# Performance work log

Hardware: AMD Instinct MI355X
Metric: run time of the kernel (lower is better)

The kernel has to match this reference:

```python
import jax, jax.numpy as jnp
import numpy as np

H = 1024      # hidden_size
I = 2048      # intermediate_size
E = 32        # num_routed_experts
B, S = 4, 2048


def setup_inputs() -> dict:
    key = jax.random.key(0)
    ks = jax.random.split(key, 8)
    scale = 0.02
    inp = {
        "hidden_states": jax.random.normal(ks[0], (B, S, H), dtype=jnp.float32),
        # router gate: stored [H, E] so logits = x @ gate_w
        "gate_w": jax.random.normal(ks[1], (H, E), dtype=jnp.float32) * scale,
        # shared SwiGLU (num_shared_experts=1), weights stored [in, out]
        "shared_gate_w": jax.random.normal(ks[2], (H, I), dtype=jnp.float32) * scale,
        "shared_up_w": jax.random.normal(ks[3], (H, I), dtype=jnp.float32) * scale,
        "shared_down_w": jax.random.normal(ks[4], (I, H), dtype=jnp.float32) * scale,
        # routed grouped SwiGLU, weights stored [E, in, out] (matches GroupedLinear)
        "routed_gate_w": jax.random.normal(ks[5], (E, H, I), dtype=jnp.float32) * scale,
        "routed_up_w": jax.random.normal(ks[6], (E, H, I), dtype=jnp.float32) * scale,
        "routed_down_w": jax.random.normal(ks[7], (E, I, H), dtype=jnp.float32) * scale,
    }
    return inp


def _grouped_mm(a, w, group_sizes):
    # a: [T, in], w: [E, in, out], group_sizes: [E] int32 -> [T, out]
    return jax.lax.ragged_dot(a, w, group_sizes)


def _swiglu(x, gw, uw, dw):
    return (jax.nn.silu(x @ gw) * (x @ uw)) @ dw


def reference(hidden_states, gate_w, shared_gate_w, shared_up_w, shared_down_w,
              routed_gate_w, routed_up_w, routed_down_w):
    b, s, h = hidden_states.shape
    x = hidden_states.reshape(-1, h)                      # [T, H]

    # ---- shared expert ----
    shared_out = _swiglu(x, shared_gate_w, shared_up_w, shared_down_w)

    # ---- router: top-1 ----
    logits = x @ gate_w                                   # [T, E]
    topk_ids = jnp.argmax(logits, axis=-1)                # [T]
    topk_val = jnp.max(logits, axis=-1)                   # [T]
    scores = jax.nn.sigmoid(topk_val)[:, None]            # [T, 1]
    xs = x * scores                                       # scale tokens by router score

    # ---- dispatch: sort tokens by expert id ----
    tokens_per_expert = jnp.zeros((E,), jnp.int32).at[topk_ids].add(1)
    order = jnp.argsort(topk_ids)                         # token ids sorted by expert
    sorted_x = xs[order]                                  # [T, H]

    # ---- grouped SwiGLU experts ----
    g = _grouped_mm(sorted_x, routed_gate_w, tokens_per_expert)   # [T, I]
    u = _grouped_mm(sorted_x, routed_up_w, tokens_per_expert)     # [T, I]
    d = _grouped_mm(jax.nn.silu(g) * u, routed_down_w, tokens_per_expert)  # [T, H]

    # ---- combine: unsort back to token order ----
    inv = jnp.argsort(order)
    routed_out = d[inv]

    return (shared_out + routed_out).reshape(b, s, h)
```

## Files before the change

kernel.cpp:

```cpp
#include <hip/hip_runtime.h>
#include <stdint.h>
#include <stddef.h>

#define TOK 8192
#define H 1024
#define IDIM 2048
#define NE 32
#define BM 128
#define BK 64
#define MAX_TILES 96

typedef __attribute__((ext_vector_type(8))) short short8;
typedef __attribute__((ext_vector_type(4))) float f32x4;
typedef __attribute__((ext_vector_type(4))) float float4v;
typedef __attribute__((ext_vector_type(4))) unsigned int uint4v;


__device__ __forceinline__ unsigned short f2bf(float x) {
  unsigned u = __builtin_bit_cast(unsigned, x);
  u += 0x7fffu + ((u >> 16) & 1u);
  return (unsigned short)(u >> 16);
}

__device__ __forceinline__ unsigned cvtpk(float lo, float hi) {
  unsigned r;
  asm("v_cvt_pk_bf16_f32 %0, %1, %2" : "=v"(r) : "v"(lo), "v"(hi));
  return r;
}

__device__ __forceinline__ void gll16(const void* g, void* l) {
  __builtin_amdgcn_global_load_lds(
      (const __attribute__((address_space(1))) unsigned int*)g,
      (__attribute__((address_space(3))) unsigned int*)l, 16, 0, 0);
}

__device__ __forceinline__ f32x4 mfma16(short8 a, short8 b, f32x4 c) {
  return __builtin_amdgcn_mfma_f32_16x16x32_bf16(a, b, c, 0, 0, 0);
}


__global__ __launch_bounds__(256) void tconv_kernel(
    const float* __restrict__ src0, unsigned short* __restrict__ dst0,
    int K, int N)
{
  __shared__ float t[64][65];
  const size_t mat = (size_t)K * N;
  const float* src = src0 + (size_t)blockIdx.z * mat;
  unsigned short* dst = dst0 + (size_t)blockIdx.z * mat;
  const int k0 = blockIdx.x * 64, n0 = blockIdx.y * 64;
  const int tid = threadIdx.x;
  {
    const int r = tid >> 4;
    const int c = (tid & 15) * 4;
    #pragma unroll
    for (int i = 0; i < 4; ++i) {
      float4v v = *(const float4v*)(src + (size_t)(k0 + r + i * 16) * N + (n0 + c));
      t[r + i * 16][c + 0] = v[0];
      t[r + i * 16][c + 1] = v[1];
      t[r + i * 16][c + 2] = v[2];
      t[r + i * 16][c + 3] = v[3];
    }
  }
  __syncthreads();
  {
    const int n = tid >> 2;
    const int kc = (tid & 3) * 16;
    uint4v o0, o1;
    #pragma unroll
    for (int q = 0; q < 4; ++q) {
      o0[q] = cvtpk(t[kc + 2 * q][n],     t[kc + 2 * q + 1][n]);
      o1[q] = cvtpk(t[kc + 8 + 2 * q][n], t[kc + 8 + 2 * q + 1][n]);
    }
    unsigned short* dp = dst + (size_t)(n0 + n) * K + (k0 + kc);
    *(uint4v*)dp = o0;
    *(uint4v*)(dp + 8) = o1;
  }
}


__global__ __launch_bounds__(256) void router_kernel(
    const float* __restrict__ x, const float* __restrict__ gw,
    unsigned short* __restrict__ xbf, unsigned short* __restrict__ xsbf,
    int* __restrict__ expert_id, int* __restrict__ counts)
{
  __shared__ float xl[8 * H];
  __shared__ float plog[8][8][NE];
  __shared__ float sscore[8];
  const int tid = threadIdx.x;
  const long t0 = (long)blockIdx.x * 8;

  const float4v* src = (const float4v*)(x + t0 * H);
  float4v* dst = (float4v*)xl;
  #pragma unroll
  for (int i = 0; i < 8; ++i) dst[tid + i * 256] = src[tid + i * 256];
  __syncthreads();

  {
    const int e = tid & 31, c = tid >> 5;
    float acc[8] = {0, 0, 0, 0, 0, 0, 0, 0};
    const float* gp = gw + (c * 128) * NE + e;
    for (int h = 0; h < 128; ++h) {
      float g = gp[h * NE];
      const float* xr = xl + (c * 128 + h);
      #pragma unroll
      for (int tk = 0; tk < 8; ++tk) acc[tk] += xr[tk * H] * g;
    }
    #pragma unroll
    for (int tk = 0; tk < 8; ++tk) plog[c][tk][e] = acc[tk];
  }
  __syncthreads();
  {
    const int e = tid & 31, tok = tid >> 5;
    float lg = 0.f;
    #pragma unroll
    for (int c = 0; c < 8; ++c) lg += plog[c][tok][e];
    float m = lg; int be = e;
    #pragma unroll
    for (int mask = 16; mask >= 1; mask >>= 1) {
      float om = __shfl_xor(m, mask);
      int   oe = __shfl_xor(be, mask);
      if (om > m || (om == m && oe < be)) { m = om; be = oe; }
    }
    if (e == 0) {
      sscore[tok] = 1.f / (1.f + __expf(-m));
      expert_id[t0 + tok] = be;
      atomicAdd(&counts[be], 1);
    }
  }
  __syncthreads();
  {
    const float sc = sscore[tid >> 5];
    const int base = (tid >> 5) * H + (tid & 31) * 32;
    #pragma unroll
    for (int i = 0; i < 4; ++i) {
      uint4v vx, vs;
      #pragma unroll
      for (int q = 0; q < 4; ++q) {
        const float a = xl[base + i * 8 + 2 * q];
        const float b = xl[base + i * 8 + 2 * q + 1];
        vx[q] = cvtpk(a, b);
        vs[q] = cvtpk(a * sc, b * sc);
      }
      *(uint4v*)(xbf  + t0 * H + base + i * 8) = vx;
      *(uint4v*)(xsbf + t0 * H + base + i * 8) = vs;
    }
  }
}


__global__ void scan_kernel(const int* __restrict__ counts, int* __restrict__ offsets,
                            int* __restrict__ cursor, int* __restrict__ tile_e,
                            int* __restrict__ tile_p, int* __restrict__ n_tiles)
{
  if (threadIdx.x != 0) return;
  int off = 0, nt = 0;
  for (int e = 0; e < NE; ++e) {
    offsets[e] = off; cursor[e] = off;
    int cc = counts[e];
    for (int k = 0; k < cc; k += BM) { tile_e[nt] = e; tile_p[nt] = off + k; ++nt; }
    off += cc;
  }
  offsets[NE] = off;
  n_tiles[0] = nt;
}


__global__ __launch_bounds__(256) void perm_kernel(
    const int* __restrict__ expert_id, int* __restrict__ cursor, int* __restrict__ perm)
{
  int t = blockIdx.x * 256 + threadIdx.x;
  int e = expert_id[t];
  int pos = atomicAdd(&cursor[e], 1);
  perm[pos] = t;
}


template<bool ROUTED>
__global__ __launch_bounds__(256, 4) void gu_kernel(
    const unsigned short* __restrict__ A,
    const unsigned short* __restrict__ GT,
    const unsigned short* __restrict__ UT,
    unsigned short* __restrict__ act,
    const int* __restrict__ perm, const int* __restrict__ tile_e,
    const int* __restrict__ tile_p, const int* __restrict__ offsets,
    const int* __restrict__ n_tiles)
{
  __shared__ short Al[BM * BK];
  __shared__ short Gl[64 * BK];
  __shared__ short Ul[64 * BK];

  const int tid = threadIdx.x;
  const int wave = tid >> 6, lane = tid & 63;
  const int wm = wave >> 1, wn = wave & 1;

  int row0, row_end;
  const unsigned short *Gt, *Ut;
  if constexpr (ROUTED) {
    if ((int)blockIdx.x >= *n_tiles) return;
    const int e = tile_e[blockIdx.x];
    row0 = tile_p[blockIdx.x];
    row_end = offsets[e + 1];
    Gt = GT + (size_t)e * H * IDIM;
    Ut = UT + (size_t)e * H * IDIM;
  } else {
    row0 = blockIdx.x * BM; row_end = row0 + BM;
    Gt = GT; Ut = UT;
  }
  const int n0 = blockIdx.y * 64;

  const unsigned short* asrc[4];
  int aoff[4];
  #pragma unroll
  for (int i = 0; i < 4; ++i) {
    const int r = wave * 32 + i * 8 + (lane >> 3);
    int p = row0 + r;
    if (ROUTED && p >= row_end) p = row0;
    int arow = p;
    if constexpr (ROUTED) arow = perm[p];
    const int cb = ((lane & 7) * 16) ^ ((r & 7) << 4);
    asrc[i] = A + (size_t)arow * H + (cb >> 1);
    aoff[i] = (wave * 32 + i * 8) * BK;
  }
  const unsigned short *gsrc[2], *usrc[2];
  int boff[2];
  #pragma unroll
  for (int i = 0; i < 2; ++i) {
    const int r = wave * 16 + i * 8 + (lane >> 3);
    const int cb = ((lane & 7) * 16) ^ ((r & 7) << 4);
    gsrc[i] = Gt + (size_t)(n0 + r) * H + (cb >> 1);
    usrc[i] = Ut + (size_t)(n0 + r) * H + (cb >> 1);
    boff[i] = (wave * 16 + i * 8) * BK;
  }

  f32x4 accg[4][2] = {};
  f32x4 accu[4][2] = {};

  #pragma unroll 1
  for (int kt = 0; kt < H / BK; ++kt) {
    __syncthreads();
    #pragma unroll
    for (int i = 0; i < 4; ++i) gll16(asrc[i] + kt * BK, Al + aoff[i]);
    #pragma unroll
    for (int i = 0; i < 2; ++i) gll16(gsrc[i] + kt * BK, Gl + boff[i]);
    #pragma unroll
    for (int i = 0; i < 2; ++i) gll16(usrc[i] + kt * BK, Ul + boff[i]);
    __syncthreads();

    #pragma unroll
    for (int kk = 0; kk < 2; ++kk) {
      short8 af[4];
      #pragma unroll
      for (int m = 0; m < 4; ++m) {
        const int r = wm * 64 + m * 16 + (lane & 15);
        const int cb = (kk * 64 + ((lane >> 4) * 16)) ^ ((r & 7) << 4);
        af[m] = *(const short8*)((const char*)Al + r * 128 + cb);
      }
      #pragma unroll
      for (int nf = 0; nf < 2; ++nf) {
        const int n = wn * 32 + nf * 16 + (lane & 15);
        const int cb = (kk * 64 + ((lane >> 4) * 16)) ^ ((n & 7) << 4);
        short8 bg = *(const short8*)((const char*)Gl + n * 128 + cb);
        short8 bu = *(const short8*)((const char*)Ul + n * 128 + cb);
        #pragma unroll
        for (int m = 0; m < 4; ++m) {
          accg[m][nf] = mfma16(af[m], bg, accg[m][nf]);
          accu[m][nf] = mfma16(af[m], bu, accu[m][nf]);
        }
      }
    }
  }

  #pragma unroll
  for (int m = 0; m < 4; ++m)
    #pragma unroll
    for (int nf = 0; nf < 2; ++nf) {
      const int col = n0 + wn * 32 + nf * 16 + (lane & 15);
      #pragma unroll
      for (int j = 0; j < 4; ++j) {
        const int row = row0 + wm * 64 + m * 16 + ((lane >> 4) * 4) + j;
        if (ROUTED && row >= row_end) continue;
        const float g = accg[m][nf][j];
        const float u = accu[m][nf][j];
        const float v = (g / (1.f + __expf(-g))) * u;
        act[(size_t)row * IDIM + col] = f2bf(v);
      }
    }
}


template<bool ROUTED>
__global__ __launch_bounds__(256, 4) void dn_kernel(
    const unsigned short* __restrict__ A,
    const unsigned short* __restrict__ DT,
    float* __restrict__ out,
    const int* __restrict__ perm, const int* __restrict__ tile_e,
    const int* __restrict__ tile_p, const int* __restrict__ offsets,
    const int* __restrict__ n_tiles)
{
  __shared__ short Al[BM * BK];
  __shared__ short Dl[128 * BK];

  const int tid = threadIdx.x;
  const int wave = tid >> 6, lane = tid & 63;
  const int wm = wave >> 1, wn = wave & 1;

  int row0, row_end;
  const unsigned short* Dt;
  if constexpr (ROUTED) {
    if ((int)blockIdx.x >= *n_tiles) return;
    const int e = tile_e[blockIdx.x];
    row0 = tile_p[blockIdx.x];
    row_end = offsets[e + 1];
    Dt = DT + (size_t)e * H * IDIM;
  } else {
    row0 = blockIdx.x * BM; row_end = row0 + BM;
    Dt = DT;
  }
  const int n0 = blockIdx.y * 128;

  const unsigned short *asrc[4], *dsrc[4];
  int soff[4];
  #pragma unroll
  for (int i = 0; i < 4; ++i) {
    const int r = wave * 32 + i * 8 + (lane >> 3);
    int p = row0 + r;
    if (ROUTED && p >= row_end) p = row0;
    const int cb = ((lane & 7) * 16) ^ ((r & 7) << 4);
    asrc[i] = A  + (size_t)p * IDIM + (cb >> 1);
    dsrc[i] = Dt + (size_t)(n0 + r) * IDIM + (cb >> 1);
    soff[i] = (wave * 32 + i * 8) * BK;
  }

  f32x4 acc[4][4] = {};

  #pragma unroll 1
  for (int kt = 0; kt < IDIM / BK; ++kt) {
    __syncthreads();
    #pragma unroll
    for (int i = 0; i < 4; ++i) gll16(asrc[i] + kt * BK, Al + soff[i]);
    #pragma unroll
    for (int i = 0; i < 4; ++i) gll16(dsrc[i] + kt * BK, Dl + soff[i]);
    __syncthreads();

    #pragma unroll
    for (int kk = 0; kk < 2; ++kk) {
      short8 af[4];
      #pragma unroll
      for (int m = 0; m < 4; ++m) {
        const int r = wm * 64 + m * 16 + (lane & 15);
        const int cb = (kk * 64 + ((lane >> 4) * 16)) ^ ((r & 7) << 4);
        af[m] = *(const short8*)((const char*)Al + r * 128 + cb);
      }
      #pragma unroll
      for (int nf = 0; nf < 4; ++nf) {
        const int n = wn * 64 + nf * 16 + (lane & 15);
        const int cb = (kk * 64 + ((lane >> 4) * 16)) ^ ((n & 7) << 4);
        short8 bd = *(const short8*)((const char*)Dl + n * 128 + cb);
        #pragma unroll
        for (int m = 0; m < 4; ++m) acc[m][nf] = mfma16(af[m], bd, acc[m][nf]);
      }
    }
  }

  #pragma unroll
  for (int m = 0; m < 4; ++m)
    #pragma unroll
    for (int nf = 0; nf < 4; ++nf) {
      const int col = n0 + wn * 64 + nf * 16 + (lane & 15);
      #pragma unroll
      for (int j = 0; j < 4; ++j) {
        const int row = row0 + wm * 64 + m * 16 + ((lane >> 4) * 4) + j;
        const float v = acc[m][nf][j];
        if constexpr (ROUTED) {
          if (row < row_end) {
            const int t = perm[row];
            out[(size_t)t * H + col] += v;
          }
        } else {
          out[(size_t)row * H + col] = v;
        }
      }
    }
}


extern "C" void kernel_launch(void* const* d_in, const int* in_sizes, int n_in,
                              void* d_out, int out_size, void* d_ws, size_t ws_size,
                              hipStream_t stream) {
  (void)in_sizes; (void)n_in; (void)out_size; (void)ws_size;
  const float* x      = (const float*)d_in[0];
  const float* gate_w = (const float*)d_in[1];
  const float* sgw    = (const float*)d_in[2];
  const float* suw    = (const float*)d_in[3];
  const float* sdw    = (const float*)d_in[4];
  const float* rgw    = (const float*)d_in[5];
  const float* ruw    = (const float*)d_in[6];
  const float* rdw    = (const float*)d_in[7];
  float* out = (float*)d_out;

  char* ws = (char*)d_ws;
  unsigned short* xbf  = (unsigned short*)(ws + 0);
  unsigned short* xsbf = (unsigned short*)(ws + 16777216);
  unsigned short* act  = (unsigned short*)(ws + 33554432);
  int* perm      = (int*)(ws + 67108864);
  int* expert_id = (int*)(ws + 67141632);
  int* counts    = (int*)(ws + 67174400);
  int* offsets   = (int*)(ws + 67174528);
  int* cursor    = (int*)(ws + 67174784);
  int* tile_e    = (int*)(ws + 67174912);
  int* tile_p    = (int*)(ws + 67175424);
  int* n_tiles   = (int*)(ws + 67175936);
  unsigned short* rgwT = (unsigned short*)(ws + 68157440);
  unsigned short* ruwT = (unsigned short*)(ws + 202375168);
  unsigned short* rdwT = (unsigned short*)(ws + 336592896);
  unsigned short* sgwT = (unsigned short*)(ws + 470810624);
  unsigned short* suwT = (unsigned short*)(ws + 475004928);
  unsigned short* sdwT = (unsigned short*)(ws + 479199232);

  hipMemsetAsync(counts, 0, NE * sizeof(int), stream);

  router_kernel<<<TOK / 8, 256, 0, stream>>>(x, gate_w, xbf, xsbf, expert_id, counts);
  scan_kernel<<<1, 64, 0, stream>>>(counts, offsets, cursor, tile_e, tile_p, n_tiles);
  perm_kernel<<<TOK / 256, 256, 0, stream>>>(expert_id, cursor, perm);

  tconv_kernel<<<dim3(H / 64, IDIM / 64, 1), 256, 0, stream>>>(sgw, sgwT, H, IDIM);
  tconv_kernel<<<dim3(H / 64, IDIM / 64, 1), 256, 0, stream>>>(suw, suwT, H, IDIM);
  tconv_kernel<<<dim3(IDIM / 64, H / 64, 1), 256, 0, stream>>>(sdw, sdwT, IDIM, H);
  gu_kernel<false><<<dim3(TOK / BM, IDIM / 64), 256, 0, stream>>>(
      xbf, sgwT, suwT, act, perm, tile_e, tile_p, offsets, n_tiles);
  dn_kernel<false><<<dim3(TOK / BM, H / 128), 256, 0, stream>>>(
      act, sdwT, out, perm, tile_e, tile_p, offsets, n_tiles);

  tconv_kernel<<<dim3(H / 64, IDIM / 64, NE), 256, 0, stream>>>(rgw, rgwT, H, IDIM);
  tconv_kernel<<<dim3(H / 64, IDIM / 64, NE), 256, 0, stream>>>(ruw, ruwT, H, IDIM);
  gu_kernel<true><<<dim3(MAX_TILES, IDIM / 64), 256, 0, stream>>>(
      xsbf, rgwT, ruwT, act, perm, tile_e, tile_p, offsets, n_tiles);
  tconv_kernel<<<dim3(IDIM / 64, H / 64, NE), 256, 0, stream>>>(rdw, rdwT, IDIM, H);
  dn_kernel<true><<<dim3(MAX_TILES, H / 128), 256, 0, stream>>>(
      act, rdwT, out, perm, tile_e, tile_p, offsets, n_tiles);
}
```

Measured before the change: 659.4 us.

## Double-buffer LDS tiles in gate/up and down GEMM kernels

Both expert GEMM kernels now keep two LDS buffers and issue the global-to-LDS load for the next K tile before the MFMA work on the current one. This overlaps memory latency with compute and drops one barrier per iteration. In exchange LDS use doubles and the launch-bounds occupancy hint falls from 4 to 2 blocks per CU. Correctness relies on gll16 completing before the single barrier at the end of each iteration.

After: 842.9 us. +27.8%, slower.

```diff
diff --git a/kernel.cpp b/kernel.cpp
--- a/kernel.cpp
+++ b/kernel.cpp
@@ -176,7 +176,7 @@
 
 
 template<bool ROUTED>
-__global__ __launch_bounds__(256, 4) void gu_kernel(
+__global__ __launch_bounds__(256, 2) void gu_kernel(
     const unsigned short* __restrict__ A,
     const unsigned short* __restrict__ GT,
     const unsigned short* __restrict__ UT,
@@ -185,9 +185,9 @@
     const int* __restrict__ tile_p, const int* __restrict__ offsets,
     const int* __restrict__ n_tiles)
 {
-  __shared__ short Al[BM * BK];
-  __shared__ short Gl[64 * BK];
-  __shared__ short Ul[64 * BK];
+  __shared__ short Al[2][BM * BK];
+  __shared__ short Gl[2][64 * BK];
+  __shared__ short Ul[2][64 * BK];
 
   const int tid = threadIdx.x;
   const int wave = tid >> 6, lane = tid & 63;
@@ -235,17 +235,18 @@
   f32x4 accg[4][2] = {};
   f32x4 accu[4][2] = {};
 
-  #pragma unroll 1
-  for (int kt = 0; kt < H / BK; ++kt) {
-    __syncthreads();
-    #pragma unroll
-    for (int i = 0; i < 4; ++i) gll16(asrc[i] + kt * BK, Al + aoff[i]);
-    #pragma unroll
-    for (int i = 0; i < 2; ++i) gll16(gsrc[i] + kt * BK, Gl + boff[i]);
-    #pragma unroll
-    for (int i = 0; i < 2; ++i) gll16(usrc[i] + kt * BK, Ul + boff[i]);
-    __syncthreads();
-
+  auto stage = [&](int kt, int buf) {
+    #pragma unroll
+    for (int i = 0; i < 4; ++i) gll16(asrc[i] + kt * BK, Al[buf] + aoff[i]);
+    #pragma unroll
+    for (int i = 0; i < 2; ++i) gll16(gsrc[i] + kt * BK, Gl[buf] + boff[i]);
+    #pragma unroll
+    for (int i = 0; i < 2; ++i) gll16(usrc[i] + kt * BK, Ul[buf] + boff[i]);
+  };
+  auto compute = [&](int buf) {
+    const char* ab = (const char*)Al[buf];
+    const char* gb = (const char*)Gl[buf];
+    const char* ub = (const char*)Ul[buf];
     #pragma unroll
     for (int kk = 0; kk < 2; ++kk) {
       short8 af[4];
@@ -253,14 +254,14 @@
       for (int m = 0; m < 4; ++m) {
         const int r = wm * 64 + m * 16 + (lane & 15);
         const int cb = (kk * 64 + ((lane >> 4) * 16)) ^ ((r & 7) << 4);
-        af[m] = *(const short8*)((const char*)Al + r * 128 + cb);
+        af[m] = *(const short8*)(ab + r * 128 + cb);
       }
       #pragma unroll
       for (int nf = 0; nf < 2; ++nf) {
         const int n = wn * 32 + nf * 16 + (lane & 15);
         const int cb = (kk * 64 + ((lane >> 4) * 16)) ^ ((n & 7) << 4);
-        short8 bg = *(const short8*)((const char*)Gl + n * 128 + cb);
-        short8 bu = *(const short8*)((const char*)Ul + n * 128 + cb);
+        short8 bg = *(const short8*)(gb + n * 128 + cb);
+        short8 bu = *(const short8*)(ub + n * 128 + cb);
         #pragma unroll
         for (int m = 0; m < 4; ++m) {
           accg[m][nf] = mfma16(af[m], bg, accg[m][nf]);
@@ -268,7 +269,19 @@
         }
       }
     }
-  }
+  };
+
+  stage(0, 0);
+  __syncthreads();
+  int cur = 0;
+  #pragma unroll 1
+  for (int kt = 0; kt < H / BK - 1; ++kt) {
+    stage(kt + 1, cur ^ 1);
+    compute(cur);
+    __syncthreads();
+    cur ^= 1;
+  }
+  compute(cur);
 
   #pragma unroll
   for (int m = 0; m < 4; ++m)
@@ -289,7 +302,7 @@
 
 
 template<bool ROUTED>
-__global__ __launch_bounds__(256, 4) void dn_kernel(
+__global__ __launch_bounds__(256, 2) void dn_kernel(
     const unsigned short* __restrict__ A,
     const unsigned short* __restrict__ DT,
     float* __restrict__ out,
@@ -297,8 +310,8 @@
     const int* __restrict__ tile_p, const int* __restrict__ offsets,
     const int* __restrict__ n_tiles)
 {
-  __shared__ short Al[BM * BK];
-  __shared__ short Dl[128 * BK];
+  __shared__ short Al[2][BM * BK];
+  __shared__ short Dl[2][128 * BK];
 
   const int tid = threadIdx.x;
   const int wave = tid >> 6, lane = tid & 63;
@@ -333,15 +346,15 @@
 
   f32x4 acc[4][4] = {};
 
-  #pragma unroll 1
-  for (int kt = 0; kt < IDIM / BK; ++kt) {
-    __syncthreads();
-    #pragma unroll
-    for (int i = 0; i < 4; ++i) gll16(asrc[i] + kt * BK, Al + soff[i]);
-    #pragma unroll
-    for (int i = 0; i < 4; ++i) gll16(dsrc[i] + kt * BK, Dl + soff[i]);
-    __syncthreads();
-
+  auto stage = [&](int kt, int buf) {
+    #pragma unroll
+    for (int i = 0; i < 4; ++i) gll16(asrc[i] + kt * BK, Al[buf] + soff[i]);
+    #pragma unroll
+    for (int i = 0; i < 4; ++i) gll16(dsrc[i] + kt * BK, Dl[buf] + soff[i]);
+  };
+  auto compute = [&](int buf) {
+    const char* ab = (const char*)Al[buf];
+    const char* db = (const char*)Dl[buf];
     #pragma unroll
     for (int kk = 0; kk < 2; ++kk) {
       short8 af[4];
@@ -349,18 +362,30 @@
       for (int m = 0; m < 4; ++m) {
         const int r = wm * 64 + m * 16 + (lane & 15);
         const int cb = (kk * 64 + ((lane >> 4) * 16)) ^ ((r & 7) << 4);
-        af[m] = *(const short8*)((const char*)Al + r * 128 + cb);
+        af[m] = *(const short8*)(ab + r * 128 + cb);
       }
       #pragma unroll
       for (int nf = 0; nf < 4; ++nf) {
         const int n = wn * 64 + nf * 16 + (lane & 15);
         const int cb = (kk * 64 + ((lane >> 4) * 16)) ^ ((n & 7) << 4);
-        short8 bd = *(const short8*)((const char*)Dl + n * 128 + cb);
+        short8 bd = *(const short8*)(db + n * 128 + cb);
         #pragma unroll
         for (int m = 0; m < 4; ++m) acc[m][nf] = mfma16(af[m], bd, acc[m][nf]);
       }
     }
-  }
+  };
+
+  stage(0, 0);
+  __syncthreads();
+  int cur = 0;
+  #pragma unroll 1
+  for (int kt = 0; kt < IDIM / BK - 1; ++kt) {
+    stage(kt + 1, cur ^ 1);
+    compute(cur);
+    __syncthreads();
+    cur ^= 1;
+  }
+  compute(cur);
 
   #pragma unroll
   for (int m = 0; m < 4; ++m)
```
